# Performance work log

Measured on AMD Instinct MI355X. Metric: run time of the kernel, lower is better.

Reference implementation:

```python
import jax, jax.numpy as jnp
import numpy as np

CONTACT_THRESHOLD = 0.5
DEFAULT_LEN = 0.1
EPS = 1e-6


def _orthonormalize(m):
    # Gram-Schmidt on rows -> proper rotation matrices, vectorized over leading dims
    a1 = m[..., 0, :]
    a2 = m[..., 1, :]
    b1 = a1 / jnp.linalg.norm(a1, axis=-1, keepdims=True)
    a2p = a2 - jnp.sum(b1 * a2, axis=-1, keepdims=True) * b1
    b2 = a2p / jnp.linalg.norm(a2p, axis=-1, keepdims=True)
    b3 = jnp.cross(b1, b2)
    return jnp.stack([b1, b2, b3], axis=-2)


def setup_inputs() -> dict:
    key = jax.random.key(0)
    k1, k2, k3, k4 = jax.random.split(key, 4)
    B, T = 512, 4096
    pred_hand_contact_prob = jax.random.uniform(k1, (B, T, 2), dtype=jnp.float32)
    pred_hand_positions = jax.random.normal(k2, (B, T, 2, 3), dtype=jnp.float32)
    obj_rotm = _orthonormalize(jax.random.normal(k3, (B, T, 3, 3), dtype=jnp.float32))
    obj_trans_init = jax.random.normal(k4, (B, 3), dtype=jnp.float32)
    return {
        'pred_hand_contact_prob': pred_hand_contact_prob,
        'pred_hand_positions': pred_hand_positions,
        'obj_rotm': obj_rotm,
        'obj_trans_init': obj_trans_init,
    }


def _fk_obj_trans(contact_prob, hand_pos, obj_rotm, obj_trans_init):
    B, T, _ = contact_prob.shape
    dtype = hand_pos.dtype
    lc = contact_prob[..., 0] > CONTACT_THRESHOLD  # [B,T]
    rc = contact_prob[..., 1] > CONTACT_THRESHOLD
    t0 = jnp.zeros((B, 1), bool)  # frame 0 forced no-contact
    ls = jnp.concatenate([t0, lc[:, 1:] & ~lc[:, :-1]], axis=1)
    rs = jnp.concatenate([t0, rc[:, 1:] & ~rc[:, :-1]], axis=1)
    lc = jnp.concatenate([t0, lc[:, 1:]], axis=1)
    rc = jnp.concatenate([t0, rc[:, 1:]], axis=1)
    z_unit = jnp.array([0.0, 0.0, 1.0], dtype=dtype)
    bidx = jnp.arange(B)

    def step(carry, xs):
        current, obj_pos, dir_local, dist = carry  # [B] int32, [B,3], [B,3], [B]
        l_c, r_c, l_s, r_s, hands, R = xs  # hands [B,2,3], R [B,3,3]
        new = jnp.where(l_s, 0, jnp.where(r_s, 1, -1))
        has_contact = ((current == 0) & l_c) | ((current == 1) & r_c)
        has_other = ((current == 0) & r_c) | ((current == 1) & l_c)
        grab = (new != -1) | (~has_contact & has_other)
        cur_grab = jnp.where(new != -1, new, 1 - current)
        release = ~grab & ~has_contact & (current != -1)
        new_current = jnp.where(grab, cur_grab, jnp.where(release, -1, current))
        # grab: recompute local direction + distance from previous obj_pos
        hand0 = hands[bidx, jnp.clip(cur_grab, 0, 1)]  # [B,3]
        vec = obj_pos - hand0
        d0 = jnp.linalg.norm(vec, axis=-1)
        valid = d0 > EPS
        unit = jnp.where(valid[:, None], vec / jnp.maximum(d0, EPS)[:, None], z_unit)
        d0 = jnp.where(valid, d0, jnp.asarray(DEFAULT_LEN, dtype))
        dir_new = jnp.einsum('bij,bi->bj', R, unit)  # R^T @ unit
        dir_local = jnp.where(grab[:, None], dir_new, dir_local)
        dist = jnp.where(grab, d0, dist)
        # attached: obj_pos = hand + R @ dir_local * dist
        attached = new_current != -1
        hand_cur = hands[bidx, jnp.clip(new_current, 0, 1)]
        new_pos = hand_cur + jnp.einsum('bij,bj->bi', R, dir_local) * dist[:, None]
        obj_pos = jnp.where(attached[:, None], new_pos, obj_pos)
        return (new_current, obj_pos, dir_local, dist), obj_pos

    carry0 = (jnp.full((B,), -1, jnp.int32),
              obj_trans_init.astype(dtype),
              jnp.zeros((B, 3), dtype),
              jnp.zeros((B,), dtype))
    xs = (lc.T, rc.T, ls.T, rs.T,
          jnp.swapaxes(hand_pos, 0, 1),
          jnp.swapaxes(obj_rotm, 0, 1))
    _, out = jax.lax.scan(step, carry0, xs)  # out [T,B,3]
    return jnp.swapaxes(out, 0, 1)  # [B,T,3]


def reference(pred_hand_contact_prob, pred_hand_positions, obj_rotm, obj_trans_init):
    return _fk_obj_trans(pred_hand_contact_prob, pred_hand_positions, obj_rotm, obj_trans_init)
```

## Files before the change

kernel.cpp:

```cpp
#include <hip/hip_runtime.h>


#define FSM_ID 0x24

__device__ __forceinline__ int fsm_compose(int f, int g) {
    int r0 = (f >> (((g     ) & 3) << 1)) & 3;
    int r1 = (f >> (((g >> 2) & 3) << 1)) & 3;
    int r2 = (f >> (((g >> 4) & 3) << 1)) & 3;
    return r0 | (r1 << 2) | (r2 << 4);
}

__device__ __forceinline__ void tmap_identity(float* m, int& rp, int& rw) {
    #pragma unroll
    for (int i = 0; i < 24; ++i) m[i] = 0.f;
    m[0] = m[4] = m[8] = 1.f;
    m[12] = m[16] = m[20] = 1.f;
    rp = 0; rw = 1;
}

__device__ __forceinline__ void tmap_compose(
    const float* Lm, int Lrp, int Lrw,
    const float* Em, int Erp, int Erw,
    float* Om, int& Orp, int& Orw)
{
    {
        float EM[9], Ec[3];
        #pragma unroll
        for (int i = 0; i < 9; ++i) EM[i] = Lrp ? Em[12+i] : Em[i];
        #pragma unroll
        for (int i = 0; i < 3; ++i) Ec[i] = Lrp ? Em[21+i] : Em[9+i];
        #pragma unroll
        for (int i = 0; i < 3; ++i) {
            #pragma unroll
            for (int j = 0; j < 3; ++j)
                Om[3*i+j] = Lm[3*i]*EM[j] + Lm[3*i+1]*EM[3+j] + Lm[3*i+2]*EM[6+j];
            Om[9+i] = Lm[3*i]*Ec[0] + Lm[3*i+1]*Ec[1] + Lm[3*i+2]*Ec[2] + Lm[9+i];
        }
        Orp = Lrp ? Erw : Erp;
    }
    {
        float EM[9], Ec[3];
        #pragma unroll
        for (int i = 0; i < 9; ++i) EM[i] = Lrw ? Em[12+i] : Em[i];
        #pragma unroll
        for (int i = 0; i < 3; ++i) Ec[i] = Lrw ? Em[21+i] : Em[9+i];
        #pragma unroll
        for (int i = 0; i < 3; ++i) {
            #pragma unroll
            for (int j = 0; j < 3; ++j)
                Om[12+3*i+j] = Lm[12+3*i]*EM[j] + Lm[12+3*i+1]*EM[3+j] + Lm[12+3*i+2]*EM[6+j];
            Om[21+i] = Lm[12+3*i]*Ec[0] + Lm[12+3*i+1]*Ec[1] + Lm[12+3*i+2]*Ec[2] + Lm[21+i];
        }
        Orw = Lrw ? Erw : Erp;
    }
}

__global__ __launch_bounds__(512, 4) void fk_scan_par3(
    const float* __restrict__ prob,
    const float* __restrict__ hands,
    const float* __restrict__ rotm,
    const float* __restrict__ tinit,
    float* __restrict__ out)
{
    const int b    = blockIdx.x;
    const int c    = threadIdx.x;
    const int lane = c & 63;
    const int w    = c >> 6;

    __shared__ int   sFSM[8];
    __shared__ float sAm[8][24];
    __shared__ int   sAf[8];

    const float* prB = prob  + (size_t)b * 4096 * 2;
    const float* hdB = hands + (size_t)b * 4096 * 6;
    const float* rmB = rotm  + (size_t)b * 4096 * 9;
    float*       obB = out   + (size_t)b * 4096 * 3;

    const float4* pr4 = (const float4*)prB + c * 4;
    const float4* hd4 = (const float4*)hdB + c * 12;
    const float4* rm4 = (const float4*)rmB + c * 18;
    float4*       ob4 = (float4*)obB       + c * 6;

    unsigned lcB = 0, rcB = 0;
    #pragma unroll
    for (int i = 0; i < 4; ++i) {
        float4 v = pr4[i];
        lcB |= (unsigned)(v.x > 0.5f) << (2*i);
        rcB |= (unsigned)(v.y > 0.5f) << (2*i);
        lcB |= (unsigned)(v.z > 0.5f) << (2*i+1);
        rcB |= (unsigned)(v.w > 0.5f) << (2*i+1);
    }
    unsigned pL = 0, pR = 0;
    if (c) {
        float2 pv = *(const float2*)(prB + 16*c - 2);
        pL = pv.x > 0.5f ? 1u : 0u;
        pR = pv.y > 0.5f ? 1u : 0u;
    }
    unsigned lsB = lcB & ~((lcB << 1) | pL);
    unsigned rsB = rcB & ~((rcB << 1) | pR);
    if (c == 0) { lcB &= ~1u; rcB &= ~1u; lsB &= ~1u; rsB &= ~1u; }

    int M = FSM_ID;
    #pragma unroll
    for (int k = 0; k < 8; ++k) {
        const unsigned lc = (lcB >> k) & 1u, rc = (rcB >> k) & 1u;
        const unsigned ls = (lsB >> k) & 1u, rs = (rsB >> k) & 1u;
        const int nwi = (int)(ls | rs);
        const int nwe = ls ? 1 : 2;
        const int e0  = lc ? 1 : (rc ? 2 : 0);
        const int e1  = rc ? 2 : (lc ? 1 : 0);
        const int mt  = nwi ? nwe * 0x15 : ((e0 << 2) | (e1 << 4));
        M = fsm_compose(mt, M);
    }
    #pragma unroll
    for (int d = 1; d < 64; d <<= 1) {
        int v  = __shfl_up(M, d);
        int cc = fsm_compose(M, v);
        M = (lane >= d) ? cc : M;
    }
    if (lane == 63) sFSM[w] = M;
    __syncthreads();
    int Pf = FSM_ID;
    for (int i = 0; i < w; ++i) Pf = fsm_compose(sFSM[i], Pf);
    int Me = __shfl_up(M, 1);
    if (lane == 0) Me = FSM_ID;
    const int s_in = fsm_compose(Me, Pf) & 3;

    float Am[24]; int rp, rw;
    tmap_identity(Am, rp, rw);
    int s = s_in;
    #pragma unroll
    for (int g = 0; g < 2; ++g) {
        float rb[36], hb[24];
        #pragma unroll
        for (int j = 0; j < 9; ++j) {
            float4 v = rm4[g*9 + j];
            rb[4*j]=v.x; rb[4*j+1]=v.y; rb[4*j+2]=v.z; rb[4*j+3]=v.w;
        }
        #pragma unroll
        for (int j = 0; j < 6; ++j) {
            float4 v = hd4[g*6 + j];
            hb[4*j]=v.x; hb[4*j+1]=v.y; hb[4*j+2]=v.z; hb[4*j+3]=v.w;
        }
        #pragma unroll
        for (int j = 0; j < 4; ++j) {
            const int k = 4*g + j;
            const unsigned lc=(lcB>>k)&1u, rc=(rcB>>k)&1u;
            const unsigned ls=(lsB>>k)&1u, rs=(rsB>>k)&1u;
            const int nwi  = (int)(ls|rs);
            const int c1 = (s==1), c2 = (s==2);
            const int hasc = (c1&(int)lc)|(c2&(int)rc);
            const int haso = (c1&(int)rc)|(c2&(int)lc);
            const int grab = nwi | ((hasc^1)&haso);
            const int gi   = nwi ? (ls?0:1) : c1;
            const int new_s= grab ? gi+1 : (hasc ? s : 0);
            const float* Rk = rb + 9*j;
            const float* Hk = hb + 6*j;
            if (grab) {
                const float hx = gi?Hk[3]:Hk[0], hy = gi?Hk[4]:Hk[1], hz = gi?Hk[5]:Hk[2];
                float t[9];
                #pragma unroll
                for (int i2=0;i2<3;++i2)
                    #pragma unroll
                    for (int j2=0;j2<3;++j2)
                        t[3*i2+j2] = Rk[i2]*Am[j2] + Rk[3+i2]*Am[3+j2] + Rk[6+i2]*Am[6+j2];
                const float ex=Am[9]-hx, ey=Am[10]-hy, ez=Am[11]-hz;
                Am[21] = Rk[0]*ex + Rk[3]*ey + Rk[6]*ez;
                Am[22] = Rk[1]*ex + Rk[4]*ey + Rk[7]*ez;
                Am[23] = Rk[2]*ex + Rk[5]*ey + Rk[8]*ez;
                #pragma unroll
                for (int i2=0;i2<9;++i2) Am[12+i2] = t[i2];
                rw = rp;
            } else if (new_s) {
                const int ci = new_s - 1;
                const float hx = ci?Hk[3]:Hk[0], hy = ci?Hk[4]:Hk[1], hz = ci?Hk[5]:Hk[2];
                float t[9];
                #pragma unroll
                for (int i2=0;i2<3;++i2)
                    #pragma unroll
                    for (int j2=0;j2<3;++j2)
                        t[3*i2+j2] = Rk[3*i2]*Am[12+j2] + Rk[3*i2+1]*Am[15+j2] + Rk[3*i2+2]*Am[18+j2];
                const float e0_ = hx + Rk[0]*Am[21] + Rk[1]*Am[22] + Rk[2]*Am[23];
                const float e1_ = hy + Rk[3]*Am[21] + Rk[4]*Am[22] + Rk[5]*Am[23];
                const float e2_ = hz + Rk[6]*Am[21] + Rk[7]*Am[22] + Rk[8]*Am[23];
                #pragma unroll
                for (int i2=0;i2<9;++i2) Am[i2] = t[i2];
                Am[9]=e0_; Am[10]=e1_; Am[11]=e2_;
                rp = rw;
            }
            s = new_s;
        }
    }

    #pragma unroll 1
    for (int d = 1; d < 64; d <<= 1) {
        float Em[24];
        #pragma unroll
        for (int i = 0; i < 24; ++i) Em[i] = __shfl_up(Am[i], d);
        const int Ef = __shfl_up(rp | (rw<<1), d);
        float Om[24]; int orp, orw;
        tmap_compose(Am, rp, rw, Em, Ef&1, (Ef>>1)&1, Om, orp, orw);
        const bool act = (lane >= d);
        #pragma unroll
        for (int i = 0; i < 24; ++i) Am[i] = act ? Om[i] : Am[i];
        rp = act ? orp : rp;
        rw = act ? orw : rw;
    }
    if (lane == 63) {
        #pragma unroll
        for (int i = 0; i < 24; ++i) sAm[w][i] = Am[i];
        sAf[w] = rp | (rw<<1);
    }
    __syncthreads();
    float Pm[24]; int Prp, Prw;
    tmap_identity(Pm, Prp, Prw);
    for (int i = 0; i < w; ++i) {
        float Lm[24];
        #pragma unroll
        for (int q = 0; q < 24; ++q) Lm[q] = sAm[i][q];
        const int f = sAf[i];
        float Tm[24]; int trp, trw;
        tmap_compose(Lm, f&1, (f>>1)&1, Pm, Prp, Prw, Tm, trp, trw);
        #pragma unroll
        for (int q = 0; q < 24; ++q) Pm[q] = Tm[q];
        Prp = trp; Prw = trw;
    }
    float Xm[24];
    #pragma unroll
    for (int i = 0; i < 24; ++i) Xm[i] = __shfl_up(Am[i], 1);
    int Xf = __shfl_up(rp | (rw<<1), 1);
    int Xrp = Xf & 1, Xrw = (Xf >> 1) & 1;
    if (lane == 0) tmap_identity(Xm, Xrp, Xrw);
    float Gm[24]; int Grp, Grw;
    tmap_compose(Xm, Xrp, Xrw, Pm, Prp, Prw, Gm, Grp, Grw);

    const float p0x = tinit[3*b], p0y = tinit[3*b+1], p0z = tinit[3*b+2];
    float px, py, pz, Wx, Wy, Wz;
    if (Grp == 0) {
        px = Gm[0]*p0x + Gm[1]*p0y + Gm[2]*p0z + Gm[9];
        py = Gm[3]*p0x + Gm[4]*p0y + Gm[5]*p0z + Gm[10];
        pz = Gm[6]*p0x + Gm[7]*p0y + Gm[8]*p0z + Gm[11];
    } else { px = Gm[9]; py = Gm[10]; pz = Gm[11]; }
    if (Grw == 0) {
        Wx = Gm[12]*p0x + Gm[13]*p0y + Gm[14]*p0z + Gm[21];
        Wy = Gm[15]*p0x + Gm[16]*p0y + Gm[17]*p0z + Gm[22];
        Wz = Gm[18]*p0x + Gm[19]*p0y + Gm[20]*p0z + Gm[23];
    } else { Wx = Gm[21]; Wy = Gm[22]; Wz = Gm[23]; }

    s = s_in;
    #pragma unroll
    for (int g = 0; g < 2; ++g) {
        float rb[36], hb[24];
        #pragma unroll
        for (int j = 0; j < 9; ++j) {
            float4 v = rm4[g*9 + j];
            rb[4*j]=v.x; rb[4*j+1]=v.y; rb[4*j+2]=v.z; rb[4*j+3]=v.w;
        }
        #pragma unroll
        for (int j = 0; j < 6; ++j) {
            float4 v = hd4[g*6 + j];
            hb[4*j]=v.x; hb[4*j+1]=v.y; hb[4*j+2]=v.z; hb[4*j+3]=v.w;
        }
        float o[12];
        #pragma unroll
        for (int j = 0; j < 4; ++j) {
            const int k = 4*g + j;
            const unsigned lc=(lcB>>k)&1u, rc=(rcB>>k)&1u;
            const unsigned ls=(lsB>>k)&1u, rs=(rsB>>k)&1u;
            const int nwi  = (int)(ls|rs);
            const int c1 = (s==1), c2 = (s==2);
            const int hasc = (c1&(int)lc)|(c2&(int)rc);
            const int haso = (c1&(int)rc)|(c2&(int)lc);
            const int grab = nwi | ((hasc^1)&haso);
            const int gi   = nwi ? (ls?0:1) : c1;
            const int new_s= grab ? gi+1 : (hasc ? s : 0);
            const float* Rk = rb + 9*j;
            const float* Hk = hb + 6*j;
            if (grab) {
                const float hx = gi?Hk[3]:Hk[0], hy = gi?Hk[4]:Hk[1], hz = gi?Hk[5]:Hk[2];
                const float vx = px-hx, vy = py-hy, vz = pz-hz;
                const float d2 = vx*vx + vy*vy + vz*vz;
                if (d2 > 1e-12f) {
                    Wx = Rk[0]*vx + Rk[3]*vy + Rk[6]*vz;
                    Wy = Rk[1]*vx + Rk[4]*vy + Rk[7]*vz;
                    Wz = Rk[2]*vx + Rk[5]*vy + Rk[8]*vz;
                } else {
                    Wx = 0.1f*Rk[6]; Wy = 0.1f*Rk[7]; Wz = 0.1f*Rk[8];
                }
            }
            if (new_s) {
                const int ci = new_s - 1;
                const float hx = ci?Hk[3]:Hk[0], hy = ci?Hk[4]:Hk[1], hz = ci?Hk[5]:Hk[2];
                px = hx + Rk[0]*Wx + Rk[1]*Wy + Rk[2]*Wz;
                py = hy + Rk[3]*Wx + Rk[4]*Wy + Rk[5]*Wz;
                pz = hz + Rk[6]*Wx + Rk[7]*Wy + Rk[8]*Wz;
            }
            s = new_s;
            o[3*j+0]=px; o[3*j+1]=py; o[3*j+2]=pz;
        }
        ob4[g*3+0] = make_float4(o[0], o[1], o[2],  o[3]);
        ob4[g*3+1] = make_float4(o[4], o[5], o[6],  o[7]);
        ob4[g*3+2] = make_float4(o[8], o[9], o[10], o[11]);
    }
}

#define CT 256
__global__ __launch_bounds__(64) void fk_scan_wave(
    const float* __restrict__ prob, const float* __restrict__ hands,
    const float* __restrict__ rotm, const float* __restrict__ tinit,
    float* __restrict__ out, int B, int T)
{
    __shared__ __align__(16) float sP[CT * 2];
    __shared__ __align__(16) float sH[CT * 8];
    __shared__ __align__(16) float sR[CT * 12];
    const int b = blockIdx.x, lane = threadIdx.x;
    const float* prB = prob  + (size_t)b * T * 2;
    const float* hdB = hands + (size_t)b * T * 6;
    const float* rmB = rotm  + (size_t)b * T * 9;
    float*       obB = out   + (size_t)b * T * 3;
    float px = tinit[3*b+0], py = tinit[3*b+1], pz = tinit[3*b+2];
    float Wx = 0.f, Wy = 0.f, Wz = 0.f;
    int cur = -1, prev_l = 0, prev_r = 0;
    for (int t0 = 0; t0 < T; t0 += CT) {
        const int n = (T - t0 < CT) ? (T - t0) : CT;
        for (int i = lane; i < n * 2; i += 64) sP[i] = prB[(size_t)t0*2 + i];
        for (int i = lane; i < n * 6; i += 64) {
            int s2 = i / 6, cc = i - 6*s2; sH[8*s2+cc] = hdB[(size_t)t0*6 + i];
        }
        for (int i = lane; i < n * 9; i += 64) {
            int s2 = i / 9, cc = i - 9*s2; sR[12*s2+cc] = rmB[(size_t)t0*9 + i];
        }
        __syncthreads();
        for (int k = 0; k < n; ++k) {
            const int t = t0 + k;
            const int rl = __builtin_amdgcn_readfirstlane(sP[2*k]   > 0.5f ? 1 : 0);
            const int rr = __builtin_amdgcn_readfirstlane(sP[2*k+1] > 0.5f ? 1 : 0);
            const int nz = (t != 0) ? 1 : 0;
            const int l_c = rl & nz, r_c = rr & nz;
            const int l_s = rl & (prev_l ^ 1) & nz, r_s = rr & (prev_r ^ 1) & nz;
            prev_l = rl; prev_r = rr;
            const int nw = l_s ? 0 : (r_s ? 1 : -1);
            const int hasc = ((cur==0)&l_c) | ((cur==1)&r_c);
            const int haso = ((cur==0)&r_c) | ((cur==1)&l_c);
            const int grab = (nw != -1) | ((hasc^1)&haso);
            const int new_cur = grab ? ((nw!=-1)?nw:(1-cur))
                                     : (((hasc^1)&(cur!=-1)) ? -1 : cur);
            if (new_cur != -1) {
                const float h0x=sH[8*k+0],h0y=sH[8*k+1],h0z=sH[8*k+2];
                const float h1x=sH[8*k+3],h1y=sH[8*k+4],h1z=sH[8*k+5];
                const float R0=sR[12*k+0],R1=sR[12*k+1],R2=sR[12*k+2];
                const float R3=sR[12*k+3],R4=sR[12*k+4],R5=sR[12*k+5];
                const float R6=sR[12*k+6],R7=sR[12*k+7],R8=sR[12*k+8];
                const float hx = new_cur ? h1x : h0x;
                const float hy = new_cur ? h1y : h0y;
                const float hz = new_cur ? h1z : h0z;
                if (grab) {
                    const float vx=px-hx, vy=py-hy, vz=pz-hz;
                    const float d2 = vx*vx+vy*vy+vz*vz;
                    if (d2 > 1e-12f) {
                        Wx = R0*vx+R3*vy+R6*vz; Wy = R1*vx+R4*vy+R7*vz; Wz = R2*vx+R5*vy+R8*vz;
                    } else { Wx = 0.1f*R6; Wy = 0.1f*R7; Wz = 0.1f*R8; }
                }
                px = hx + (R0*Wx+R1*Wy+R2*Wz);
                py = hy + (R3*Wx+R4*Wy+R5*Wz);
                pz = hz + (R6*Wx+R7*Wy+R8*Wz);
            }
            cur = new_cur;
            if (lane == 0) {
                obB[3*(size_t)t+0]=px; obB[3*(size_t)t+1]=py; obB[3*(size_t)t+2]=pz;
            }
        }
        __syncthreads();
    }
}

extern "C" void kernel_launch(void* const* d_in, const int* in_sizes, int n_in,
                              void* d_out, int out_size, void* d_ws, size_t ws_size,
                              hipStream_t stream) {
    const float* prob  = (const float*)d_in[0];
    const float* hands = (const float*)d_in[1];
    const float* rotm  = (const float*)d_in[2];
    const float* tinit = (const float*)d_in[3];
    float* out = (float*)d_out;

    const int B = in_sizes[3] / 3;
    const int T = in_sizes[0] / (B * 2);

    if (T == 4096) {
        hipLaunchKernelGGL(fk_scan_par3, dim3(B), dim3(512), 0, stream,
                           prob, hands, rotm, tinit, out);
    } else {
        hipLaunchKernelGGL(fk_scan_wave, dim3(B), dim3(64), 0, stream,
                           prob, hands, rotm, tinit, out, B, T);
    }
}
```

Before: 64.99 us.

## Apply warp prefix maps to vectors instead of composing full transfer maps

The cross-wave combine stage no longer composes 24-float affine transfer maps across waves. It applies each earlier wave's map directly to the running (position, world) vector pair, turning matrix-matrix products into matrix-vector products. The intra-wave shuffle scan is fully unrolled and composes in place only on active lanes, replacing the compute-then-select pattern. The launch attributes are reexpressed as waves_per_eu(4,4). This cuts ALU work and register pressure in the scan phase, at the cost of possible lane divergence inside the unrolled scan loop.

```diff
diff --git a/kernel.cpp b/kernel.cpp
--- a/kernel.cpp
+++ b/kernel.cpp
@@ -18,10 +18,9 @@
     rp = 0; rw = 1;
 }
 
-__device__ __forceinline__ void tmap_compose(
-    const float* Lm, int Lrp, int Lrw,
-    const float* Em, int Erp, int Erw,
-    float* Om, int& Orp, int& Orw)
+__device__ __forceinline__ void tmap_compose_inplace(
+    float* Lm, int& Lrp, int& Lrw,
+    const float* Em, int Erp, int Erw)
 {
     {
         float EM[9], Ec[3];
@@ -31,12 +30,12 @@
         for (int i = 0; i < 3; ++i) Ec[i] = Lrp ? Em[21+i] : Em[9+i];
         #pragma unroll
         for (int i = 0; i < 3; ++i) {
-            #pragma unroll
-            for (int j = 0; j < 3; ++j)
-                Om[3*i+j] = Lm[3*i]*EM[j] + Lm[3*i+1]*EM[3+j] + Lm[3*i+2]*EM[6+j];
-            Om[9+i] = Lm[3*i]*Ec[0] + Lm[3*i+1]*Ec[1] + Lm[3*i+2]*Ec[2] + Lm[9+i];
-        }
-        Orp = Lrp ? Erw : Erp;
+            const float a = Lm[3*i], b = Lm[3*i+1], c = Lm[3*i+2];
+            Lm[3*i+0] = a*EM[0] + b*EM[3] + c*EM[6];
+            Lm[3*i+1] = a*EM[1] + b*EM[4] + c*EM[7];
+            Lm[3*i+2] = a*EM[2] + b*EM[5] + c*EM[8];
+            Lm[9+i]  += a*Ec[0] + b*Ec[1] + c*Ec[2];
+        }
     }
     {
         float EM[9], Ec[3];
@@ -46,16 +45,35 @@
         for (int i = 0; i < 3; ++i) Ec[i] = Lrw ? Em[21+i] : Em[9+i];
         #pragma unroll
         for (int i = 0; i < 3; ++i) {
-            #pragma unroll
-            for (int j = 0; j < 3; ++j)
-                Om[12+3*i+j] = Lm[12+3*i]*EM[j] + Lm[12+3*i+1]*EM[3+j] + Lm[12+3*i+2]*EM[6+j];
-            Om[21+i] = Lm[12+3*i]*Ec[0] + Lm[12+3*i+1]*Ec[1] + Lm[12+3*i+2]*Ec[2] + Lm[21+i];
-        }
-        Orw = Lrw ? Erw : Erp;
-    }
-}
-
-__global__ __launch_bounds__(512, 4) void fk_scan_par3(
+            const float a = Lm[12+3*i], b = Lm[12+3*i+1], c = Lm[12+3*i+2];
+            Lm[12+3*i+0] = a*EM[0] + b*EM[3] + c*EM[6];
+            Lm[12+3*i+1] = a*EM[1] + b*EM[4] + c*EM[7];
+            Lm[12+3*i+2] = a*EM[2] + b*EM[5] + c*EM[8];
+            Lm[21+i]    += a*Ec[0] + b*Ec[1] + c*Ec[2];
+        }
+    }
+    const int nrp = Lrp ? Erw : Erp;
+    const int nrw = Lrw ? Erw : Erp;
+    Lrp = nrp; Lrw = nrw;
+}
+
+__device__ __forceinline__ void tmap_apply(
+    const float* m, int rp_, int rw_,
+    const float* pin, const float* win, float* pout, float* wout)
+{
+    const float* ip = rp_ ? win : pin;
+    pout[0] = m[0]*ip[0] + m[1]*ip[1] + m[2]*ip[2] + m[9];
+    pout[1] = m[3]*ip[0] + m[4]*ip[1] + m[5]*ip[2] + m[10];
+    pout[2] = m[6]*ip[0] + m[7]*ip[1] + m[8]*ip[2] + m[11];
+    const float* iw = rw_ ? win : pin;
+    wout[0] = m[12]*iw[0] + m[13]*iw[1] + m[14]*iw[2] + m[21];
+    wout[1] = m[15]*iw[0] + m[16]*iw[1] + m[17]*iw[2] + m[22];
+    wout[2] = m[18]*iw[0] + m[19]*iw[1] + m[20]*iw[2] + m[23];
+}
+
+__global__ void __launch_bounds__(512)
+__attribute__((amdgpu_waves_per_eu(4, 4)))
+fk_scan_par4(
     const float* __restrict__ prob,
     const float* __restrict__ hands,
     const float* __restrict__ rotm,
@@ -192,19 +210,14 @@
         }
     }
 
-    #pragma unroll 1
+    #pragma unroll
     for (int d = 1; d < 64; d <<= 1) {
         float Em[24];
         #pragma unroll
         for (int i = 0; i < 24; ++i) Em[i] = __shfl_up(Am[i], d);
         const int Ef = __shfl_up(rp | (rw<<1), d);
-        float Om[24]; int orp, orw;
-        tmap_compose(Am, rp, rw, Em, Ef&1, (Ef>>1)&1, Om, orp, orw);
-        const bool act = (lane >= d);
-        #pragma unroll
-        for (int i = 0; i < 24; ++i) Am[i] = act ? Om[i] : Am[i];
-        rp = act ? orp : rp;
-        rw = act ? orw : rw;
+        if (lane >= d)
+            tmap_compose_inplace(Am, rp, rw, Em, Ef & 1, (Ef >> 1) & 1);
     }
     if (lane == 63) {
         #pragma unroll
@@ -212,40 +225,28 @@
         sAf[w] = rp | (rw<<1);
     }
     __syncthreads();
-    float Pm[24]; int Prp, Prw;
-    tmap_identity(Pm, Prp, Prw);
+
+    {
+        #pragma unroll
+        for (int i = 0; i < 24; ++i) Am[i] = __shfl_up(Am[i], 1);
+        const int t = __shfl_up(rp | (rw<<1), 1);
+        rp = t & 1; rw = (t >> 1) & 1;
+        if (lane == 0) tmap_identity(Am, rp, rw);
+    }
+
+    float vp[3] = { tinit[3*b], tinit[3*b+1], tinit[3*b+2] };
+    float vw[3] = { 0.f, 0.f, 0.f };
     for (int i = 0; i < w; ++i) {
-        float Lm[24];
-        #pragma unroll
-        for (int q = 0; q < 24; ++q) Lm[q] = sAm[i][q];
+        float np[3], nw2[3];
         const int f = sAf[i];
-        float Tm[24]; int trp, trw;
-        tmap_compose(Lm, f&1, (f>>1)&1, Pm, Prp, Prw, Tm, trp, trw);
-        #pragma unroll
-        for (int q = 0; q < 24; ++q) Pm[q] = Tm[q];
-        Prp = trp; Prw = trw;
-    }
-    float Xm[24];
-    #pragma unroll
-    for (int i = 0; i < 24; ++i) Xm[i] = __shfl_up(Am[i], 1);
-    int Xf = __shfl_up(rp | (rw<<1), 1);
-    int Xrp = Xf & 1, Xrw = (Xf >> 1) & 1;
-    if (lane == 0) tmap_identity(Xm, Xrp, Xrw);
-    float Gm[24]; int Grp, Grw;
-    tmap_compose(Xm, Xrp, Xrw, Pm, Prp, Prw, Gm, Grp, Grw);
-
-    const float p0x = tinit[3*b], p0y = tinit[3*b+1], p0z = tinit[3*b+2];
-    float px, py, pz, Wx, Wy, Wz;
-    if (Grp == 0) {
-        px = Gm[0]*p0x + Gm[1]*p0y + Gm[2]*p0z + Gm[9];
-        py = Gm[3]*p0x + Gm[4]*p0y + Gm[5]*p0z + Gm[10];
-        pz = Gm[6]*p0x + Gm[7]*p0y + Gm[8]*p0z + Gm[11];
-    } else { px = Gm[9]; py = Gm[10]; pz = Gm[11]; }
-    if (Grw == 0) {
-        Wx = Gm[12]*p0x + Gm[13]*p0y + Gm[14]*p0z + Gm[21];
-        Wy = Gm[15]*p0x + Gm[16]*p0y + Gm[17]*p0z + Gm[22];
-        Wz = Gm[18]*p0x + Gm[19]*p0y + Gm[20]*p0z + Gm[23];
-    } else { Wx = Gm[21]; Wy = Gm[22]; Wz = Gm[23]; }
+        tmap_apply(&sAm[i][0], f & 1, (f >> 1) & 1, vp, vw, np, nw2);
+        vp[0]=np[0]; vp[1]=np[1]; vp[2]=np[2];
+        vw[0]=nw2[0]; vw[1]=nw2[1]; vw[2]=nw2[2];
+    }
+    float pv[3], wv[3];
+    tmap_apply(Am, rp, rw, vp, vw, pv, wv);
+    float px = pv[0], py = pv[1], pz = pv[2];
+    float Wx = wv[0], Wy = wv[1], Wz = wv[2];
 
     s = s_in;
     #pragma unroll
@@ -387,7 +388,7 @@
     const int T = in_sizes[0] / (B * 2);
 
     if (T == 4096) {
-        hipLaunchKernelGGL(fk_scan_par3, dim3(B), dim3(512), 0, stream,
+        hipLaunchKernelGGL(fk_scan_par4, dim3(B), dim3(512), 0, stream,
                            prob, hands, rotm, tinit, out);
     } else {
         hipLaunchKernelGGL(fk_scan_wave, dim3(B), dim3(64), 0, stream,
```

Measured after the change: 81.69 us. +25.7%, slower.
